# Kernel optimization log

Hardware: AMD Instinct MI355X
Metric: run time of the kernel (lower is better)

The kernel has to match this reference:

```python
import jax, jax.numpy as jnp
import numpy as np

N, E, B, T, H, L = 8192, 2048, 512, 128, 128, 3


def setup_inputs() -> dict:
    key = jax.random.key(0)
    ks = jax.random.split(key, 14)
    # sparse binary hyperedge incidence [E, N]
    Hbat = (jax.random.uniform(ks[0], (E, N)) < 0.01).astype(jnp.float32)
    DV2 = jax.random.uniform(ks[1], (N,)) + 0.1    # D_v^{-1/2} node scaling
    invDE = jax.random.uniform(ks[2], (E,)) + 0.1  # D_e^{-1} edge scaling
    data = jax.random.randint(ks[3], (B, T), 0, N, dtype=jnp.int32)
    lens = jax.random.randint(ks[4], (B,), 1, T + 1, dtype=jnp.int32)
    data_length = jnp.sort(lens)[::-1].at[0].set(T)  # descending, max == T (pack_padded)
    poi = jax.random.normal(ks[5], (N, H), dtype=jnp.float32)
    s = 1.0 / float(np.sqrt(H))
    hgc1_w = jax.random.uniform(ks[6], (H, H), minval=-s, maxval=s)
    hgc1_b = jax.random.uniform(ks[7], (H,), minval=-s, maxval=s)
    hgc2_w = jax.random.uniform(ks[8], (H, H), minval=-s, maxval=s)
    hgc2_b = jax.random.uniform(ks[9], (H,), minval=-s, maxval=s)
    Wih = jax.random.uniform(ks[10], (L, 3 * H, H), minval=-s, maxval=s)
    Whh = jax.random.uniform(ks[11], (L, 3 * H, H), minval=-s, maxval=s)
    bih = jax.random.uniform(ks[12], (L, 3 * H), minval=-s, maxval=s)
    bhh = jax.random.uniform(ks[13], (L, 3 * H), minval=-s, maxval=s)
    return dict(Hbat=Hbat, DV2=DV2, invDE=invDE, data=data, data_length=data_length,
                poi=poi, hgc1_w=hgc1_w, hgc1_b=hgc1_b, hgc2_w=hgc2_w, hgc2_b=hgc2_b,
                Wih=Wih, Whh=Whh, bih=bih, bhh=bhh)


def _gru(x, Wih, Whh, bih, bhh):
    # torch nn.GRU (batch_first, 1 layer, h0=0). x: [B,T,H] -> [B,T,H]
    gx = jnp.einsum('bth,gh->btg', x, Wih) + bih  # precompute input gates [B,T,3H]

    def step(h, gxt):
        gh = h @ Whh.T + bhh
        xr, xz, xn = jnp.split(gxt, 3, axis=-1)
        hr, hz, hn = jnp.split(gh, 3, axis=-1)
        r = jax.nn.sigmoid(xr + hr)
        z = jax.nn.sigmoid(xz + hz)
        n = jnp.tanh(xn + r * hn)
        h_new = (1.0 - z) * n + z * h
        return h_new, h_new

    h0 = jnp.zeros((x.shape[0], x.shape[2]), x.dtype)
    _, ys = jax.lax.scan(step, h0, jnp.swapaxes(gx, 0, 1))
    return jnp.swapaxes(ys, 0, 1)


def reference(Hbat, DV2, invDE, data, data_length, poi,
              hgc1_w, hgc1_b, hgc2_w, hgc2_b, Wih, Whh, bih, bhh):
    # G = diag(DV2) Hbat^T diag(invDE) Hbat diag(DV2); diag_embed GEMMs == row/col scaling
    G = (DV2[:, None] * Hbat.T) @ (invDE[:, None] * Hbat * DV2[None, :])  # [N,N]
    x = jax.nn.relu(G @ (poi @ hgc1_w + hgc1_b)) + poi
    x = G @ (x @ hgc2_w + hgc2_b)
    batch_emb = x[data]  # [B,T,H]
    Tn = batch_emb.shape[1]
    # pad_packed_sequence zero-fills beyond each sequence's length
    mask = (jnp.arange(Tn)[None, :] < data_length[:, None])[:, :, None].astype(batch_emb.dtype)
    inp = batch_emb
    n_layers = Wih.shape[0]
    for l in range(n_layers - 1):
        out = _gru(inp, Wih[l], Whh[l], bih[l], bhh[l]) * mask
        inp = batch_emb + jax.nn.relu(out)
    out = _gru(inp, Wih[-1], Whh[-1], bih[-1], bhh[-1]) * mask
    last = out[jnp.arange(out.shape[0]), data_length - 1]  # gather last valid step
    return jnp.tanh(last)
```

## Files before the change

kernel.cpp:

```cpp
#include <hip/hip_runtime.h>

#define NN 8192
#define EE 2048
#define BB 512
#define TT 128
#define HH 128
#define G3 384
#define MAXNNZ 256
#define MAXDEG 96

typedef __attribute__((ext_vector_type(8))) _Float16 f16x8;
typedef __attribute__((ext_vector_type(4))) float f32x4;

__device__ __forceinline__ float sigm(float x){ return 1.0f/(1.0f+__expf(-x)); }
__device__ __forceinline__ float tanhfast(float x){ return 2.0f/(1.0f+__expf(-2.0f*x)) - 1.0f; }

__device__ __forceinline__ void bar_lds(){
  __builtin_amdgcn_sched_barrier(0);
  asm volatile("s_waitcnt lgkmcnt(0)\n\ts_barrier" ::: "memory");
  __builtin_amdgcn_sched_barrier(0);
}

__global__ __launch_bounds__(256)
void build_nnz(const float* __restrict__ Hb, int* __restrict__ idx, int* __restrict__ cnt){
  __shared__ int c;
  const int e = blockIdx.x;
  if (threadIdx.x == 0) c = 0;
  __syncthreads();
  const float* row = Hb + (size_t)e * NN;
  for (int n = threadIdx.x; n < NN; n += 256){
    if (row[n] != 0.0f){
      int p = atomicAdd(&c, 1);
      if (p < MAXNNZ) idx[e*MAXNNZ + p] = n;
    }
  }
  __syncthreads();
  if (threadIdx.x == 0) cnt[e] = (c < MAXNNZ ? c : MAXNNZ);
}

__global__ __launch_bounds__(128)
void build_nodelists(const int* __restrict__ idx, const int* __restrict__ cnt,
                     int* __restrict__ ndeg, int* __restrict__ nidx){
  const int e = blockIdx.x;
  const int c = cnt[e];
  for (int k = threadIdx.x; k < c; k += 128){
    int n = idx[e*MAXNNZ + k];
    int p = atomicAdd(&ndeg[n], 1);
    if (p < MAXDEG) nidx[n*MAXDEG + p] = e;
  }
}

__global__ __launch_bounds__(256)
void prep_w(const float* __restrict__ W, _Float16* __restrict__ whi,
            _Float16* __restrict__ wlo, int n){
  int i = blockIdx.x*256 + threadIdx.x;
  if (i >= n) return;
  float g = W[i] * 16.0f;
  _Float16 h = (_Float16)g;
  whi[i] = h;
  wlo[i] = (_Float16)(g - (float)h);
}

__global__ __launch_bounds__(256)
void prep_split(const float* __restrict__ X, _Float16* __restrict__ hi,
                _Float16* __restrict__ lo, int n){
  int i = blockIdx.x*256 + threadIdx.x;
  if (i >= n) return;
  float v = X[i];
  _Float16 h = (_Float16)v;
  hi[i] = h;
  lo[i] = (_Float16)(v - (float)h);
}

__global__ __launch_bounds__(256)
void prep_wt(const float* __restrict__ W, _Float16* __restrict__ wt_hi,
             _Float16* __restrict__ wt_lo){
  int i = blockIdx.x*256 + threadIdx.x;
  int k = i >> 7, j = i & 127;
  float g = W[i] * 16.0f;
  _Float16 h = (_Float16)g;
  wt_hi[j*HH + k] = h;
  wt_lo[j*HH + k] = (_Float16)(g - (float)h);
}

template<bool SCALE>
__global__ __launch_bounds__(256)
void mm128_mfma(const _Float16* __restrict__ Ahi, const _Float16* __restrict__ Alo,
                const _Float16* __restrict__ Bh, const _Float16* __restrict__ Bl,
                const float* __restrict__ bias, const float* __restrict__ rowscale,
                float* __restrict__ C)
{
  const int tid = threadIdx.x;
  const int w = tid >> 6, l = tid & 63;
  const int lm = l & 15, q = l >> 4;
  const int r0 = blockIdx.x * 32;
  const int n0 = w * 32;

  f32x4 acc[2][2];
  #pragma unroll
  for (int m=0;m<2;m++)
    #pragma unroll
    for (int n=0;n<2;n++) acc[m][n] = (f32x4){0.f,0.f,0.f,0.f};

  #pragma unroll 2
  for (int ks = 0; ks < 4; ++ks){
    const int kb = ks*32 + q*8;
    f16x8 ah[2], al[2];
    #pragma unroll
    for (int m=0;m<2;m++){
      const size_t ro = (size_t)(r0 + m*16 + lm)*HH + kb;
      ah[m] = *(const f16x8*)(Ahi + ro);
      al[m] = *(const f16x8*)(Alo + ro);
    }
    #pragma unroll
    for (int n=0;n<2;n++){
      const int j = n0 + n*16 + lm;
      f16x8 bh = *(const f16x8*)(Bh + (size_t)j*HH + kb);
      f16x8 bl = *(const f16x8*)(Bl + (size_t)j*HH + kb);
      #pragma unroll
      for (int m=0;m<2;m++){
        acc[m][n] = __builtin_amdgcn_mfma_f32_16x16x32_f16(ah[m], bh, acc[m][n], 0,0,0);
        acc[m][n] = __builtin_amdgcn_mfma_f32_16x16x32_f16(al[m], bh, acc[m][n], 0,0,0);
        acc[m][n] = __builtin_amdgcn_mfma_f32_16x16x32_f16(ah[m], bl, acc[m][n], 0,0,0);
      }
    }
  }
  #pragma unroll
  for (int n=0;n<2;n++){
    const int j = n0 + n*16 + lm;
    const float bv = bias[j];
    #pragma unroll
    for (int m=0;m<2;m++){
      #pragma unroll
      for (int i=0;i<4;i++){
        int r = r0 + m*16 + q*4 + i;
        float cv = acc[m][n][i]*(1.0f/16.0f) + bv;
        if (SCALE) cv *= rowscale[r];
        C[(size_t)r*HH + j] = cv;
      }
    }
  }
}

__global__ __launch_bounds__(128)
void edge_gather(const float* __restrict__ Xs, const int* __restrict__ idx,
                 const int* __restrict__ cnt, const float* __restrict__ invDE,
                 float* __restrict__ Eb){
  __shared__ int sidx[MAXNNZ];
  const int e = blockIdx.x, h = threadIdx.x;
  const int c = cnt[e];
  for (int k = h; k < c; k += 128) sidx[k] = idx[e*MAXNNZ + k];
  __syncthreads();
  float acc = 0.0f;
  int k = 0;
  for (; k + 4 <= c; k += 4){
    float a0 = Xs[(size_t)sidx[k+0]*HH + h];
    float a1 = Xs[(size_t)sidx[k+1]*HH + h];
    float a2 = Xs[(size_t)sidx[k+2]*HH + h];
    float a3 = Xs[(size_t)sidx[k+3]*HH + h];
    acc += (a0 + a1) + (a2 + a3);
  }
  for (; k < c; ++k) acc += Xs[(size_t)sidx[k]*HH + h];
  Eb[e*HH + h] = invDE[e] * acc;
}

template<int MODE>
__global__ __launch_bounds__(128)
void node_gather(const float* __restrict__ Eb, const int* __restrict__ nidx,
                 const int* __restrict__ ndeg, const float* __restrict__ DV2,
                 const float* __restrict__ poi, _Float16* __restrict__ ohi,
                 _Float16* __restrict__ olo, float* __restrict__ Xo){
  __shared__ int sidx[MAXDEG];
  const int n = blockIdx.x, h = threadIdx.x;
  int c = ndeg[n]; c = c < MAXDEG ? c : MAXDEG;
  for (int k = h; k < c; k += 128) sidx[k] = nidx[n*MAXDEG + k];
  __syncthreads();
  float acc = 0.0f;
  int k = 0;
  for (; k + 4 <= c; k += 4){
    float a0 = Eb[(size_t)sidx[k+0]*HH + h];
    float a1 = Eb[(size_t)sidx[k+1]*HH + h];
    float a2 = Eb[(size_t)sidx[k+2]*HH + h];
    float a3 = Eb[(size_t)sidx[k+3]*HH + h];
    acc += (a0 + a1) + (a2 + a3);
  }
  for (; k < c; ++k) acc += Eb[(size_t)sidx[k]*HH + h];
  float v = DV2[n] * acc;
  if (MODE == 1){
    float val = fmaxf(v, 0.0f) + poi[(size_t)n*HH + h];
    _Float16 hh = (_Float16)val;
    ohi[(size_t)n*HH + h] = hh;
    olo[(size_t)n*HH + h] = (_Float16)(val - (float)hh);
  } else {
    Xo[(size_t)n*HH + h] = v;
  }
}

__global__ __launch_bounds__(256)
void gather_emb(const float* __restrict__ X, const int* __restrict__ data,
                float* __restrict__ emb, _Float16* __restrict__ aHi,
                _Float16* __restrict__ aLo){
  int r = blockIdx.x*2 + (threadIdx.x >> 7);
  int h = threadIdx.x & 127;
  int n = data[r];
  float v = X[(size_t)n*HH + h];
  size_t o = (size_t)r*HH + h;
  emb[o] = v;
  _Float16 hh = (_Float16)v;
  aHi[o] = hh;
  aLo[o] = (_Float16)(v - (float)hh);
}

__global__ __launch_bounds__(256)
void gx_gemm(const _Float16* __restrict__ Ahi, const _Float16* __restrict__ Alo,
             const _Float16* __restrict__ Whi, const _Float16* __restrict__ Wlo,
             const float* __restrict__ bih, const int* __restrict__ lens,
             float* __restrict__ gx)
{
  const int blk = blockIdx.x;
  const int b = blk >> 2, tt = blk & 3;
  const int lenb = lens[b];
  if (tt*32 >= lenb) return;
  const int tid = threadIdx.x;
  const int w = tid >> 6, l = tid & 63;
  const int lm = l & 15, q = l >> 4;
  const int r0 = b*TT + tt*32;
  const int n0 = w*96;

  f32x4 acc[2][6];
  #pragma unroll
  for (int m=0;m<2;m++)
    #pragma unroll
    for (int n=0;n<6;n++) acc[m][n] = (f32x4){0.f,0.f,0.f,0.f};

  #pragma unroll 2
  for (int ks = 0; ks < 4; ++ks){
    const int kb = ks*32 + q*8;
    f16x8 ah[2], al[2];
    #pragma unroll
    for (int m=0;m<2;m++){
      const size_t ro = (size_t)(r0 + m*16 + lm)*HH + kb;
      ah[m] = *(const f16x8*)(Ahi + ro);
      al[m] = *(const f16x8*)(Alo + ro);
    }
    #pragma unroll
    for (int n=0;n<6;n++){
      const int g = n0 + n*16 + lm;
      f16x8 bh = *(const f16x8*)(Whi + (size_t)g*HH + kb);
      f16x8 bl = *(const f16x8*)(Wlo + (size_t)g*HH + kb);
      #pragma unroll
      for (int m=0;m<2;m++){
        acc[m][n] = __builtin_amdgcn_mfma_f32_16x16x32_f16(ah[m], bh, acc[m][n], 0,0,0);
        acc[m][n] = __builtin_amdgcn_mfma_f32_16x16x32_f16(al[m], bh, acc[m][n], 0,0,0);
        acc[m][n] = __builtin_amdgcn_mfma_f32_16x16x32_f16(ah[m], bl, acc[m][n], 0,0,0);
      }
    }
  }
  #pragma unroll
  for (int n=0;n<6;n++){
    const int g = n0 + n*16 + lm;
    const float bv = bih[g];
    #pragma unroll
    for (int m=0;m<2;m++){
      #pragma unroll
      for (int i=0;i<4;i++){
        int t = tt*32 + m*16 + q*4 + i;
        gx[((size_t)b*TT + t)*G3 + g] = acc[m][n][i]*(1.0f/16.0f) + bv;
      }
    }
  }
}

template<bool FINAL>
__global__ __launch_bounds__(512, 1)
void gru_scan3(const float* __restrict__ gxp, const float* __restrict__ Whh,
               const float* __restrict__ bhh, const int* __restrict__ lens,
               const float* __restrict__ emb, _Float16* __restrict__ aHi,
               _Float16* __restrict__ aLo, float* __restrict__ final_out)
{
  __shared__ _Float16 hbuf[2][16*HH];
  __shared__ float ghT[2][392];
  const int tid = threadIdx.x;
  const int w = tid >> 6, lane = tid & 63;
  const int lm = lane & 15, q = lane >> 4;
  const int b0 = blockIdx.x * 2;

  f16x8 wf[3][4];
  #pragma unroll
  for (int n=0; n<3; ++n){
    const int col = w*48 + n*16 + lm;
    const float* wr = Whh + (size_t)col*HH;
    #pragma unroll
    for (int ks=0; ks<4; ++ks){
      const int kb = ks*32 + q*8;
      float4 f0 = *(const float4*)(wr + kb);
      float4 f1 = *(const float4*)(wr + kb + 4);
      float fv[8] = {f0.x,f0.y,f0.z,f0.w,f1.x,f1.y,f1.z,f1.w};
      union { f16x8 v; _Float16 u[8]; } uu;
      #pragma unroll
      for (int j=0;j<8;j++) uu.u[j] = (_Float16)(fv[j] * 16.0f);
      wf[n][ks] = uu.v;
    }
  }
  const float S = 1.0f/16.0f;
  const int lenmax = lens[b0];

  const int gb = tid >> 7, gd = tid & 127;
  float bR=0.f, bZ=0.f, bN=0.f; int glen=0;
  const float* gxrow = nullptr;
  const float* erow = nullptr;
  _Float16 *ahrow = nullptr, *alrow = nullptr;
  if (tid < 256){
    bR = bhh[gd]; bZ = bhh[HH+gd]; bN = bhh[2*HH+gd];
    glen = lens[b0+gb];
    gxrow = gxp + (size_t)(b0+gb)*TT*G3;
    if (!FINAL){
      erow  = emb + (size_t)(b0+gb)*TT*HH + gd;
      ahrow = aHi + (size_t)(b0+gb)*TT*HH + gd;
      alrow = aLo + (size_t)(b0+gb)*TT*HH + gd;
    }
  }

  {
    unsigned int* z = (unsigned int*)&hbuf[0][0];
    #pragma unroll 1
    for (int i = tid; i < 2*16*HH/2; i += 512) z[i] = 0u;
  }
  __syncthreads();

  float xv0=0.f, xv1=0.f, xv2=0.f, xe=0.f, hp=0.f;
  if (tid < 256){
    xv0 = gxrow[gd]; xv1 = gxrow[128+gd]; xv2 = gxrow[256+gd];
    if (!FINAL) xe = erow[0];
  }

  int cur = 0;
  #pragma unroll 1
  for (int t = 0; t < lenmax; ++t){
    f16x8 av[4];
    #pragma unroll
    for (int ks=0; ks<4; ++ks){
      int off = (lm*256 + ks*64 + q*16) ^ ((lm & 7) << 4);
      av[ks] = *(const f16x8*)((const char*)&hbuf[cur][0] + off);
    }
    float xn0=0.f, xn1=0.f, xn2=0.f, xen=0.f;
    if (tid < 256){
      int tp = (t+1 < lenmax) ? t+1 : t;
      const float* bgx = gxrow + (size_t)tp*G3;
      xn0 = bgx[gd]; xn1 = bgx[128+gd]; xn2 = bgx[256+gd];
      if (!FINAL) xen = erow[(size_t)tp*HH];
    }
    f32x4 a0 = (f32x4){0.f,0.f,0.f,0.f}, a1 = a0, a2 = a0;
    #pragma unroll
    for (int ks=0; ks<4; ++ks){
      a0 = __builtin_amdgcn_mfma_f32_16x16x32_f16(av[ks], wf[0][ks], a0, 0,0,0);
      a1 = __builtin_amdgcn_mfma_f32_16x16x32_f16(av[ks], wf[1][ks], a1, 0,0,0);
      a2 = __builtin_amdgcn_mfma_f32_16x16x32_f16(av[ks], wf[2][ks], a2, 0,0,0);
    }
    if (q == 0){
      const int c0 = w*48 + lm;
      ghT[0][c0]      = a0[0];  ghT[1][c0]      = a0[1];
      ghT[0][c0+16]   = a1[0];  ghT[1][c0+16]   = a1[1];
      ghT[0][c0+32]   = a2[0];  ghT[1][c0+32]   = a2[1];
    }
    bar_lds();

    if (tid < 256){
      float gr = ghT[gb][gd], gz = ghT[gb][128+gd], gn = ghT[gb][256+gd];
      float r = sigm(xv0 + gr*S + bR);
      float z = sigm(xv1 + gz*S + bZ);
      float n = tanhfast(xv2 + r*(gn*S + bN));
      float hnew = (1.0f - z)*n + z*hp;
      hp = hnew;
      int off = (gb*256 + gd*2) ^ (gb << 4);
      *(_Float16*)((char*)&hbuf[cur^1][0] + off) = (_Float16)hnew;
      if (!FINAL){
        float a = xe + fmaxf(hnew, 0.0f);
        _Float16 ah = (_Float16)a;
        ahrow[(size_t)t*HH] = ah;
        alrow[(size_t)t*HH] = (_Float16)(a - (float)ah);
      } else {
        if (t == glen - 1)
          final_out[(size_t)(b0+gb)*HH + gd] = tanhfast(hnew);
      }
    }
    xv0 = xn0; xv1 = xn1; xv2 = xn2; xe = xen;
    bar_lds();
    cur ^= 1;
  }
}

extern "C" void kernel_launch(void* const* d_in, const int* in_sizes, int n_in,
                              void* d_out, int out_size, void* d_ws, size_t ws_size,
                              hipStream_t stream)
{
  const float* Hb    = (const float*)d_in[0];
  const float* DV2   = (const float*)d_in[1];
  const float* invDE = (const float*)d_in[2];
  const int*   data  = (const int*)d_in[3];
  const int*   dlen  = (const int*)d_in[4];
  const float* poi   = (const float*)d_in[5];
  const float* w1    = (const float*)d_in[6];
  const float* b1    = (const float*)d_in[7];
  const float* w2    = (const float*)d_in[8];
  const float* b2    = (const float*)d_in[9];
  const float* Wih   = (const float*)d_in[10];
  const float* Whh   = (const float*)d_in[11];
  const float* bih   = (const float*)d_in[12];
  const float* bhh   = (const float*)d_in[13];
  float* out = (float*)d_out;

  float* ws   = (float*)d_ws;
  float* x1s  = ws;
  float* x3s  = x1s + (size_t)NN*HH;
  float* x4   = x3s + (size_t)NN*HH;
  float* ebuf = x4  + (size_t)NN*HH;
  float* gx   = ebuf + (size_t)EE*HH;
  float* emb  = gx  + (size_t)BB*TT*G3;
  _Float16* aHi  = (_Float16*)(emb + (size_t)BB*TT*HH);
  _Float16* aLo  = aHi + (size_t)BB*TT*HH;
  _Float16* x2hi = aLo + (size_t)BB*TT*HH;
  _Float16* x2lo = x2hi + (size_t)NN*HH;
  _Float16* pHi  = x2lo + (size_t)NN*HH;
  _Float16* pLo  = pHi + (size_t)NN*HH;
  _Float16* Whi  = pLo + (size_t)NN*HH;
  _Float16* Wlo  = Whi + (size_t)3*G3*HH;
  _Float16* w1th = Wlo + (size_t)3*G3*HH;
  _Float16* w1tl = w1th + (size_t)HH*HH;
  _Float16* w2th = w1tl + (size_t)HH*HH;
  _Float16* w2tl = w2th + (size_t)HH*HH;
  int* idx  = (int*)(w2tl + (size_t)HH*HH);
  int* cnt  = idx + (size_t)EE*MAXNNZ;
  int* ndeg = cnt + EE;
  int* nidx = ndeg + NN;

  hipMemsetAsync(ndeg, 0, NN*sizeof(int), stream);
  build_nnz<<<EE, 256, 0, stream>>>(Hb, idx, cnt);
  build_nodelists<<<EE, 128, 0, stream>>>(idx, cnt, ndeg, nidx);
  prep_w<<<(3*G3*HH + 255)/256, 256, 0, stream>>>(Wih, Whi, Wlo, 3*G3*HH);
  prep_wt<<<HH*HH/256, 256, 0, stream>>>(w1, w1th, w1tl);
  prep_wt<<<HH*HH/256, 256, 0, stream>>>(w2, w2th, w2tl);
  prep_split<<<NN*HH/256, 256, 0, stream>>>(poi, pHi, pLo, NN*HH);

  mm128_mfma<true><<<NN/32, 256, 0, stream>>>(pHi, pLo, w1th, w1tl, b1, DV2, x1s);
  edge_gather<<<EE, 128, 0, stream>>>(x1s, idx, cnt, invDE, ebuf);
  node_gather<1><<<NN, 128, 0, stream>>>(ebuf, nidx, ndeg, DV2, poi, x2hi, x2lo, (float*)nullptr);
  mm128_mfma<true><<<NN/32, 256, 0, stream>>>(x2hi, x2lo, w2th, w2tl, b2, DV2, x3s);
  edge_gather<<<EE, 128, 0, stream>>>(x3s, idx, cnt, invDE, ebuf);
  node_gather<2><<<NN, 128, 0, stream>>>(ebuf, nidx, ndeg, DV2, (const float*)nullptr,
                                         (_Float16*)nullptr, (_Float16*)nullptr, x4);
  gather_emb<<<BB*TT/2, 256, 0, stream>>>(x4, data, emb, aHi, aLo);

  for (int l = 0; l < 3; ++l){
    gx_gemm<<<BB*4, 256, 0, stream>>>(aHi, aLo, Whi + (size_t)l*G3*HH,
        Wlo + (size_t)l*G3*HH, bih + (size_t)l*G3, dlen, gx);
    if (l < 2)
      gru_scan3<false><<<BB/2, 512, 0, stream>>>(gx, Whh + (size_t)l*G3*HH,
          bhh + (size_t)l*G3, dlen, emb, aHi, aLo, (float*)nullptr);
    else
      gru_scan3<true><<<BB/2, 512, 0, stream>>>(gx, Whh + (size_t)l*G3*HH,
          bhh + (size_t)l*G3, dlen, (const float*)nullptr,
          (_Float16*)nullptr, (_Float16*)nullptr, out);
  }
}
```

Before: 580.4 us.

## Remap GRU scan columns per wave to drop LDS gate exchange barrier

The recurrent weights are remapped so each wave's three MFMA tiles hold the r, z and n gates for the same 16 hidden dims. The gate math can then run straight from the MFMA accumulators, which removes the ghT shared-memory exchange and one barrier per timestep. The final output write is deferred until after the loop. The gx GEMM is also retiled to 64 timesteps per block with a per-row length guard, trading fewer blocks for more accumulator registers.

```diff
diff --git a/kernel.cpp b/kernel.cpp
--- a/kernel.cpp
+++ b/kernel.cpp
@@ -218,27 +218,27 @@
              float* __restrict__ gx)
 {
   const int blk = blockIdx.x;
-  const int b = blk >> 2, tt = blk & 3;
+  const int b = blk >> 1, tt = blk & 1;
   const int lenb = lens[b];
-  if (tt*32 >= lenb) return;
+  if (tt*64 >= lenb) return;
   const int tid = threadIdx.x;
   const int w = tid >> 6, l = tid & 63;
   const int lm = l & 15, q = l >> 4;
-  const int r0 = b*TT + tt*32;
+  const int r0 = b*TT + tt*64;
   const int n0 = w*96;
 
-  f32x4 acc[2][6];
+  f32x4 acc[4][6];
   #pragma unroll
-  for (int m=0;m<2;m++)
+  for (int m=0;m<4;m++)
     #pragma unroll
     for (int n=0;n<6;n++) acc[m][n] = (f32x4){0.f,0.f,0.f,0.f};
 
   #pragma unroll 2
   for (int ks = 0; ks < 4; ++ks){
     const int kb = ks*32 + q*8;
-    f16x8 ah[2], al[2];
-    #pragma unroll
-    for (int m=0;m<2;m++){
+    f16x8 ah[4], al[4];
+    #pragma unroll
+    for (int m=0;m<4;m++){
       const size_t ro = (size_t)(r0 + m*16 + lm)*HH + kb;
       ah[m] = *(const f16x8*)(Ahi + ro);
       al[m] = *(const f16x8*)(Alo + ro);
@@ -249,7 +249,7 @@
       f16x8 bh = *(const f16x8*)(Whi + (size_t)g*HH + kb);
       f16x8 bl = *(const f16x8*)(Wlo + (size_t)g*HH + kb);
       #pragma unroll
-      for (int m=0;m<2;m++){
+      for (int m=0;m<4;m++){
         acc[m][n] = __builtin_amdgcn_mfma_f32_16x16x32_f16(ah[m], bh, acc[m][n], 0,0,0);
         acc[m][n] = __builtin_amdgcn_mfma_f32_16x16x32_f16(al[m], bh, acc[m][n], 0,0,0);
         acc[m][n] = __builtin_amdgcn_mfma_f32_16x16x32_f16(ah[m], bl, acc[m][n], 0,0,0);
@@ -261,11 +261,12 @@
     const int g = n0 + n*16 + lm;
     const float bv = bih[g];
     #pragma unroll
-    for (int m=0;m<2;m++){
+    for (int m=0;m<4;m++){
       #pragma unroll
       for (int i=0;i<4;i++){
-        int t = tt*32 + m*16 + q*4 + i;
-        gx[((size_t)b*TT + t)*G3 + g] = acc[m][n][i]*(1.0f/16.0f) + bv;
+        int t = tt*64 + m*16 + q*4 + i;
+        if (t < lenb)
+          gx[((size_t)b*TT + t)*G3 + g] = acc[m][n][i]*(1.0f/16.0f) + bv;
       }
     }
   }
@@ -273,23 +274,22 @@
 
 template<bool FINAL>
 __global__ __launch_bounds__(512, 1)
-void gru_scan3(const float* __restrict__ gxp, const float* __restrict__ Whh,
+void gru_scan4(const float* __restrict__ gxp, const float* __restrict__ Whh,
                const float* __restrict__ bhh, const int* __restrict__ lens,
                const float* __restrict__ emb, _Float16* __restrict__ aHi,
                _Float16* __restrict__ aLo, float* __restrict__ final_out)
 {
   __shared__ _Float16 hbuf[2][16*HH];
-  __shared__ float ghT[2][392];
   const int tid = threadIdx.x;
   const int w = tid >> 6, lane = tid & 63;
   const int lm = lane & 15, q = lane >> 4;
   const int b0 = blockIdx.x * 2;
+  const int d = w*16 + lm;
 
   f16x8 wf[3][4];
   #pragma unroll
-  for (int n=0; n<3; ++n){
-    const int col = w*48 + n*16 + lm;
-    const float* wr = Whh + (size_t)col*HH;
+  for (int g=0; g<3; ++g){
+    const float* wr = Whh + (size_t)(g*HH + d)*HH;
     #pragma unroll
     for (int ks=0; ks<4; ++ks){
       const int kb = ks*32 + q*8;
@@ -299,26 +299,22 @@
       union { f16x8 v; _Float16 u[8]; } uu;
       #pragma unroll
       for (int j=0;j<8;j++) uu.u[j] = (_Float16)(fv[j] * 16.0f);
-      wf[n][ks] = uu.v;
+      wf[g][ks] = uu.v;
     }
   }
   const float S = 1.0f/16.0f;
   const int lenmax = lens[b0];
-
-  const int gb = tid >> 7, gd = tid & 127;
-  float bR=0.f, bZ=0.f, bN=0.f; int glen=0;
-  const float* gxrow = nullptr;
-  const float* erow = nullptr;
-  _Float16 *ahrow = nullptr, *alrow = nullptr;
-  if (tid < 256){
-    bR = bhh[gd]; bZ = bhh[HH+gd]; bN = bhh[2*HH+gd];
-    glen = lens[b0+gb];
-    gxrow = gxp + (size_t)(b0+gb)*TT*G3;
-    if (!FINAL){
-      erow  = emb + (size_t)(b0+gb)*TT*HH + gd;
-      ahrow = aHi + (size_t)(b0+gb)*TT*HH + gd;
-      alrow = aLo + (size_t)(b0+gb)*TT*HH + gd;
-    }
+  const int len0 = lens[b0], len1 = lens[b0+1];
+  const float bR = bhh[d], bZ = bhh[HH+d], bN = bhh[2*HH+d];
+  const float* gx0 = gxp + (size_t)b0*TT*G3 + d;
+  const float* gx1 = gxp + (size_t)(b0+1)*TT*G3 + d;
+  const float* e0 = nullptr; const float* e1 = nullptr;
+  _Float16 *ah0=nullptr,*al0=nullptr,*ah1=nullptr,*al1=nullptr;
+  if (!FINAL){
+    e0  = emb + (size_t)b0*TT*HH + d;
+    e1  = emb + (size_t)(b0+1)*TT*HH + d;
+    ah0 = aHi + (size_t)b0*TT*HH + d;      al0 = aLo + (size_t)b0*TT*HH + d;
+    ah1 = aHi + (size_t)(b0+1)*TT*HH + d;  al1 = aLo + (size_t)(b0+1)*TT*HH + d;
   }
 
   {
@@ -328,10 +324,13 @@
   }
   __syncthreads();
 
-  float xv0=0.f, xv1=0.f, xv2=0.f, xe=0.f, hp=0.f;
-  if (tid < 256){
-    xv0 = gxrow[gd]; xv1 = gxrow[128+gd]; xv2 = gxrow[256+gd];
-    if (!FINAL) xe = erow[0];
+  float hp0=0.f, hp1=0.f, fo0=0.f, fo1=0.f;
+  float xv[6] = {0,0,0,0,0,0};
+  float xe0=0.f, xe1=0.f;
+  if (q == 0){
+    xv[0]=gx0[0]; xv[1]=gx0[128]; xv[2]=gx0[256];
+    xv[3]=gx1[0]; xv[4]=gx1[128]; xv[5]=gx1[256];
+    if (!FINAL){ xe0 = e0[0]; xe1 = e1[0]; }
   }
 
   int cur = 0;
@@ -343,50 +342,56 @@
       int off = (lm*256 + ks*64 + q*16) ^ ((lm & 7) << 4);
       av[ks] = *(const f16x8*)((const char*)&hbuf[cur][0] + off);
     }
-    float xn0=0.f, xn1=0.f, xn2=0.f, xen=0.f;
-    if (tid < 256){
+    float xn[6] = {0,0,0,0,0,0};
+    float xen0=0.f, xen1=0.f;
+    if (q == 0){
       int tp = (t+1 < lenmax) ? t+1 : t;
-      const float* bgx = gxrow + (size_t)tp*G3;
-      xn0 = bgx[gd]; xn1 = bgx[128+gd]; xn2 = bgx[256+gd];
-      if (!FINAL) xen = erow[(size_t)tp*HH];
-    }
-    f32x4 a0 = (f32x4){0.f,0.f,0.f,0.f}, a1 = a0, a2 = a0;
+      const float* g0 = gx0 + (size_t)tp*G3;
+      const float* g1 = gx1 + (size_t)tp*G3;
+      xn[0]=g0[0]; xn[1]=g0[128]; xn[2]=g0[256];
+      xn[3]=g1[0]; xn[4]=g1[128]; xn[5]=g1[256];
+      if (!FINAL){ xen0 = e0[(size_t)tp*HH]; xen1 = e1[(size_t)tp*HH]; }
+    }
+    f32x4 aR = (f32x4){0.f,0.f,0.f,0.f}, aZ = aR, aN = aR;
     #pragma unroll
     for (int ks=0; ks<4; ++ks){
-      a0 = __builtin_amdgcn_mfma_f32_16x16x32_f16(av[ks], wf[0][ks], a0, 0,0,0);
-      a1 = __builtin_amdgcn_mfma_f32_16x16x32_f16(av[ks], wf[1][ks], a1, 0,0,0);
-      a2 = __builtin_amdgcn_mfma_f32_16x16x32_f16(av[ks], wf[2][ks], a2, 0,0,0);
+      aR = __builtin_amdgcn_mfma_f32_16x16x32_f16(av[ks], wf[0][ks], aR, 0,0,0);
+      aZ = __builtin_amdgcn_mfma_f32_16x16x32_f16(av[ks], wf[1][ks], aZ, 0,0,0);
+      aN = __builtin_amdgcn_mfma_f32_16x16x32_f16(av[ks], wf[2][ks], aN, 0,0,0);
     }
     if (q == 0){
-      const int c0 = w*48 + lm;
-      ghT[0][c0]      = a0[0];  ghT[1][c0]      = a0[1];
-      ghT[0][c0+16]   = a1[0];  ghT[1][c0+16]   = a1[1];
-      ghT[0][c0+32]   = a2[0];  ghT[1][c0+32]   = a2[1];
-    }
-    bar_lds();
-
-    if (tid < 256){
-      float gr = ghT[gb][gd], gz = ghT[gb][128+gd], gn = ghT[gb][256+gd];
-      float r = sigm(xv0 + gr*S + bR);
-      float z = sigm(xv1 + gz*S + bZ);
-      float n = tanhfast(xv2 + r*(gn*S + bN));
-      float hnew = (1.0f - z)*n + z*hp;
-      hp = hnew;
-      int off = (gb*256 + gd*2) ^ (gb << 4);
-      *(_Float16*)((char*)&hbuf[cur^1][0] + off) = (_Float16)hnew;
+      float r0 = sigm(xv[0] + aR[0]*S + bR);
+      float z0 = sigm(xv[1] + aZ[0]*S + bZ);
+      float n0 = tanhfast(xv[2] + r0*(aN[0]*S + bN));
+      float h0 = (1.0f - z0)*n0 + z0*hp0; hp0 = h0;
+      float r1 = sigm(xv[3] + aR[1]*S + bR);
+      float z1 = sigm(xv[4] + aZ[1]*S + bZ);
+      float n1 = tanhfast(xv[5] + r1*(aN[1]*S + bN));
+      float h1 = (1.0f - z1)*n1 + z1*hp1; hp1 = h1;
+      char* hb = (char*)&hbuf[cur^1][0];
+      *(_Float16*)(hb + (d*2))                 = (_Float16)h0;
+      *(_Float16*)(hb + 256 + ((d*2) ^ 16))    = (_Float16)h1;
       if (!FINAL){
-        float a = xe + fmaxf(hnew, 0.0f);
-        _Float16 ah = (_Float16)a;
-        ahrow[(size_t)t*HH] = ah;
-        alrow[(size_t)t*HH] = (_Float16)(a - (float)ah);
+        float a0v = xe0 + fmaxf(h0, 0.0f);
+        _Float16 a0h = (_Float16)a0v;
+        ah0[(size_t)t*HH] = a0h;  al0[(size_t)t*HH] = (_Float16)(a0v - (float)a0h);
+        float a1v = xe1 + fmaxf(h1, 0.0f);
+        _Float16 a1h = (_Float16)a1v;
+        ah1[(size_t)t*HH] = a1h;  al1[(size_t)t*HH] = (_Float16)(a1v - (float)a1h);
       } else {
-        if (t == glen - 1)
-          final_out[(size_t)(b0+gb)*HH + gd] = tanhfast(hnew);
+        if (t == len0 - 1) fo0 = tanhfast(h0);
+        if (t == len1 - 1) fo1 = tanhfast(h1);
       }
     }
-    xv0 = xn0; xv1 = xn1; xv2 = xn2; xe = xen;
+    #pragma unroll
+    for (int k2=0;k2<6;k2++) xv[k2] = xn[k2];
+    xe0 = xen0; xe1 = xen1;
     bar_lds();
     cur ^= 1;
+  }
+  if (FINAL && q == 0){
+    final_out[(size_t)b0*HH + d]     = fo0;
+    final_out[(size_t)(b0+1)*HH + d] = fo1;
   }
 }
 
@@ -452,13 +457,13 @@
   gather_emb<<<BB*TT/2, 256, 0, stream>>>(x4, data, emb, aHi, aLo);
 
   for (int l = 0; l < 3; ++l){
-    gx_gemm<<<BB*4, 256, 0, stream>>>(aHi, aLo, Whi + (size_t)l*G3*HH,
+    gx_gemm<<<BB*2, 256, 0, stream>>>(aHi, aLo, Whi + (size_t)l*G3*HH,
         Wlo + (size_t)l*G3*HH, bih + (size_t)l*G3, dlen, gx);
     if (l < 2)
-      gru_scan3<false><<<BB/2, 512, 0, stream>>>(gx, Whh + (size_t)l*G3*HH,
+      gru_scan4<false><<<BB/2, 512, 0, stream>>>(gx, Whh + (size_t)l*G3*HH,
           bhh + (size_t)l*G3, dlen, emb, aHi, aLo, (float*)nullptr);
     else
-      gru_scan3<true><<<BB/2, 512, 0, stream>>>(gx, Whh + (size_t)l*G3*HH,
+      gru_scan4<true><<<BB/2, 512, 0, stream>>>(gx, Whh + (size_t)l*G3*HH,
           bhh + (size_t)l*G3, dlen, (const float*)nullptr,
           (_Float16*)nullptr, (_Float16*)nullptr, out);
   }
```

New measurement: 682.9 us. +17.7%, slower.

## Run GRU scan with one sequence per block and enlarge gx GEMM row tiles

Applied to the files above, without the earlier changes.

The GRU recurrent kernel now processes one batch sequence per 256-thread block instead of two per 512-thread block. Each wave holds six Whh fragments and loops only to that sequence's own length, so short sequences no longer wait on the longest in a pair, and two blocks can share a CU. The gx GEMM tile grows from 32 to 64 timesteps per block, with stores past the sequence length skipped. The costs are more registers per wave, half the MFMA rows left unused per step since only one row of the 16-row tile is live, and coarser GEMM blocks.

```diff
diff --git a/kernel.cpp b/kernel.cpp
--- a/kernel.cpp
+++ b/kernel.cpp
@@ -218,27 +218,27 @@
              float* __restrict__ gx)
 {
   const int blk = blockIdx.x;
-  const int b = blk >> 2, tt = blk & 3;
+  const int b = blk >> 1, tt = blk & 1;
   const int lenb = lens[b];
-  if (tt*32 >= lenb) return;
+  if (tt*64 >= lenb) return;
   const int tid = threadIdx.x;
   const int w = tid >> 6, l = tid & 63;
   const int lm = l & 15, q = l >> 4;
-  const int r0 = b*TT + tt*32;
+  const int r0 = b*TT + tt*64;
   const int n0 = w*96;
 
-  f32x4 acc[2][6];
+  f32x4 acc[4][6];
   #pragma unroll
-  for (int m=0;m<2;m++)
+  for (int m=0;m<4;m++)
     #pragma unroll
     for (int n=0;n<6;n++) acc[m][n] = (f32x4){0.f,0.f,0.f,0.f};
 
   #pragma unroll 2
   for (int ks = 0; ks < 4; ++ks){
     const int kb = ks*32 + q*8;
-    f16x8 ah[2], al[2];
-    #pragma unroll
-    for (int m=0;m<2;m++){
+    f16x8 ah[4], al[4];
+    #pragma unroll
+    for (int m=0;m<4;m++){
       const size_t ro = (size_t)(r0 + m*16 + lm)*HH + kb;
       ah[m] = *(const f16x8*)(Ahi + ro);
       al[m] = *(const f16x8*)(Alo + ro);
@@ -249,7 +249,7 @@
       f16x8 bh = *(const f16x8*)(Whi + (size_t)g*HH + kb);
       f16x8 bl = *(const f16x8*)(Wlo + (size_t)g*HH + kb);
       #pragma unroll
-      for (int m=0;m<2;m++){
+      for (int m=0;m<4;m++){
         acc[m][n] = __builtin_amdgcn_mfma_f32_16x16x32_f16(ah[m], bh, acc[m][n], 0,0,0);
         acc[m][n] = __builtin_amdgcn_mfma_f32_16x16x32_f16(al[m], bh, acc[m][n], 0,0,0);
         acc[m][n] = __builtin_amdgcn_mfma_f32_16x16x32_f16(ah[m], bl, acc[m][n], 0,0,0);
@@ -261,34 +261,35 @@
     const int g = n0 + n*16 + lm;
     const float bv = bih[g];
     #pragma unroll
-    for (int m=0;m<2;m++){
+    for (int m=0;m<4;m++){
       #pragma unroll
       for (int i=0;i<4;i++){
-        int t = tt*32 + m*16 + q*4 + i;
-        gx[((size_t)b*TT + t)*G3 + g] = acc[m][n][i]*(1.0f/16.0f) + bv;
+        int t = tt*64 + m*16 + q*4 + i;
+        if (t < lenb)
+          gx[((size_t)b*TT + t)*G3 + g] = acc[m][n][i]*(1.0f/16.0f) + bv;
       }
     }
   }
 }
 
 template<bool FINAL>
-__global__ __launch_bounds__(512, 1)
-void gru_scan3(const float* __restrict__ gxp, const float* __restrict__ Whh,
+__global__ __launch_bounds__(256, 2)
+void gru_scan5(const float* __restrict__ gxp, const float* __restrict__ Whh,
                const float* __restrict__ bhh, const int* __restrict__ lens,
                const float* __restrict__ emb, _Float16* __restrict__ aHi,
                _Float16* __restrict__ aLo, float* __restrict__ final_out)
 {
   __shared__ _Float16 hbuf[2][16*HH];
-  __shared__ float ghT[2][392];
+  __shared__ float ghT[G3 + 8];
   const int tid = threadIdx.x;
   const int w = tid >> 6, lane = tid & 63;
   const int lm = lane & 15, q = lane >> 4;
-  const int b0 = blockIdx.x * 2;
-
-  f16x8 wf[3][4];
+  const int b = blockIdx.x;
+
+  f16x8 wf[6][4];
   #pragma unroll
-  for (int n=0; n<3; ++n){
-    const int col = w*48 + n*16 + lm;
+  for (int n=0; n<6; ++n){
+    const int col = w*96 + n*16 + lm;
     const float* wr = Whh + (size_t)col*HH;
     #pragma unroll
     for (int ks=0; ks<4; ++ks){
@@ -303,40 +304,39 @@
     }
   }
   const float S = 1.0f/16.0f;
-  const int lenmax = lens[b0];
-
-  const int gb = tid >> 7, gd = tid & 127;
-  float bR=0.f, bZ=0.f, bN=0.f; int glen=0;
+  const int lenb = lens[b];
+
+  const int gd = tid & 127;
+  float bR=0.f, bZ=0.f, bN=0.f;
   const float* gxrow = nullptr;
   const float* erow = nullptr;
   _Float16 *ahrow = nullptr, *alrow = nullptr;
-  if (tid < 256){
+  if (tid < 128){
     bR = bhh[gd]; bZ = bhh[HH+gd]; bN = bhh[2*HH+gd];
-    glen = lens[b0+gb];
-    gxrow = gxp + (size_t)(b0+gb)*TT*G3;
+    gxrow = gxp + (size_t)b*TT*G3;
     if (!FINAL){
-      erow  = emb + (size_t)(b0+gb)*TT*HH + gd;
-      ahrow = aHi + (size_t)(b0+gb)*TT*HH + gd;
-      alrow = aLo + (size_t)(b0+gb)*TT*HH + gd;
+      erow  = emb + (size_t)b*TT*HH + gd;
+      ahrow = aHi + (size_t)b*TT*HH + gd;
+      alrow = aLo + (size_t)b*TT*HH + gd;
     }
   }
 
   {
     unsigned int* z = (unsigned int*)&hbuf[0][0];
     #pragma unroll 1
-    for (int i = tid; i < 2*16*HH/2; i += 512) z[i] = 0u;
+    for (int i = tid; i < 2*16*HH/2; i += 256) z[i] = 0u;
   }
   __syncthreads();
 
-  float xv0=0.f, xv1=0.f, xv2=0.f, xe=0.f, hp=0.f;
-  if (tid < 256){
+  float xv0=0.f, xv1=0.f, xv2=0.f, xe=0.f, hp=0.f, fo=0.f;
+  if (tid < 128){
     xv0 = gxrow[gd]; xv1 = gxrow[128+gd]; xv2 = gxrow[256+gd];
     if (!FINAL) xe = erow[0];
   }
 
   int cur = 0;
   #pragma unroll 1
-  for (int t = 0; t < lenmax; ++t){
+  for (int t = 0; t < lenb; ++t){
     f16x8 av[4];
     #pragma unroll
     for (int ks=0; ks<4; ++ks){
@@ -344,50 +344,51 @@
       av[ks] = *(const f16x8*)((const char*)&hbuf[cur][0] + off);
     }
     float xn0=0.f, xn1=0.f, xn2=0.f, xen=0.f;
-    if (tid < 256){
-      int tp = (t+1 < lenmax) ? t+1 : t;
+    if (tid < 128){
+      int tp = (t+1 < lenb) ? t+1 : t;
       const float* bgx = gxrow + (size_t)tp*G3;
       xn0 = bgx[gd]; xn1 = bgx[128+gd]; xn2 = bgx[256+gd];
       if (!FINAL) xen = erow[(size_t)tp*HH];
     }
-    f32x4 a0 = (f32x4){0.f,0.f,0.f,0.f}, a1 = a0, a2 = a0;
+    f32x4 a[6];
+    #pragma unroll
+    for (int n=0;n<6;n++) a[n] = (f32x4){0.f,0.f,0.f,0.f};
     #pragma unroll
     for (int ks=0; ks<4; ++ks){
-      a0 = __builtin_amdgcn_mfma_f32_16x16x32_f16(av[ks], wf[0][ks], a0, 0,0,0);
-      a1 = __builtin_amdgcn_mfma_f32_16x16x32_f16(av[ks], wf[1][ks], a1, 0,0,0);
-      a2 = __builtin_amdgcn_mfma_f32_16x16x32_f16(av[ks], wf[2][ks], a2, 0,0,0);
+      #pragma unroll
+      for (int n=0;n<6;n++)
+        a[n] = __builtin_amdgcn_mfma_f32_16x16x32_f16(av[ks], wf[n][ks], a[n], 0,0,0);
     }
     if (q == 0){
-      const int c0 = w*48 + lm;
-      ghT[0][c0]      = a0[0];  ghT[1][c0]      = a0[1];
-      ghT[0][c0+16]   = a1[0];  ghT[1][c0+16]   = a1[1];
-      ghT[0][c0+32]   = a2[0];  ghT[1][c0+32]   = a2[1];
+      const int c0 = w*96 + lm;
+      #pragma unroll
+      for (int n=0;n<6;n++) ghT[c0 + n*16] = a[n][0];
     }
     bar_lds();
 
-    if (tid < 256){
-      float gr = ghT[gb][gd], gz = ghT[gb][128+gd], gn = ghT[gb][256+gd];
+    if (tid < 128){
+      float gr = ghT[gd], gz = ghT[128+gd], gn = ghT[256+gd];
       float r = sigm(xv0 + gr*S + bR);
       float z = sigm(xv1 + gz*S + bZ);
       float n = tanhfast(xv2 + r*(gn*S + bN));
       float hnew = (1.0f - z)*n + z*hp;
       hp = hnew;
-      int off = (gb*256 + gd*2) ^ (gb << 4);
-      *(_Float16*)((char*)&hbuf[cur^1][0] + off) = (_Float16)hnew;
+      *(_Float16*)((char*)&hbuf[cur^1][0] + gd*2) = (_Float16)hnew;
       if (!FINAL){
-        float a = xe + fmaxf(hnew, 0.0f);
-        _Float16 ah = (_Float16)a;
+        float av_ = xe + fmaxf(hnew, 0.0f);
+        _Float16 ah = (_Float16)av_;
         ahrow[(size_t)t*HH] = ah;
-        alrow[(size_t)t*HH] = (_Float16)(a - (float)ah);
+        alrow[(size_t)t*HH] = (_Float16)(av_ - (float)ah);
       } else {
-        if (t == glen - 1)
-          final_out[(size_t)(b0+gb)*HH + gd] = tanhfast(hnew);
+        if (t == lenb - 1) fo = tanhfast(hnew);
       }
     }
     xv0 = xn0; xv1 = xn1; xv2 = xn2; xe = xen;
     bar_lds();
     cur ^= 1;
   }
+  if (FINAL && tid < 128)
+    final_out[(size_t)b*HH + gd] = fo;
 }
 
 extern "C" void kernel_launch(void* const* d_in, const int* in_sizes, int n_in,
@@ -452,13 +453,13 @@
   gather_emb<<<BB*TT/2, 256, 0, stream>>>(x4, data, emb, aHi, aLo);
 
   for (int l = 0; l < 3; ++l){
-    gx_gemm<<<BB*4, 256, 0, stream>>>(aHi, aLo, Whi + (size_t)l*G3*HH,
+    gx_gemm<<<BB*2, 256, 0, stream>>>(aHi, aLo, Whi + (size_t)l*G3*HH,
         Wlo + (size_t)l*G3*HH, bih + (size_t)l*G3, dlen, gx);
     if (l < 2)
-      gru_scan3<false><<<BB/2, 512, 0, stream>>>(gx, Whh + (size_t)l*G3*HH,
+      gru_scan5<false><<<BB, 256, 0, stream>>>(gx, Whh + (size_t)l*G3*HH,
           bhh + (size_t)l*G3, dlen, emb, aHi, aLo, (float*)nullptr);
     else
-      gru_scan3<true><<<BB/2, 512, 0, stream>>>(gx, Whh + (size_t)l*G3*HH,
+      gru_scan5<true><<<BB, 256, 0, stream>>>(gx, Whh + (size_t)l*G3*HH,
           bhh + (size_t)l*G3, dlen, (const float*)nullptr,
           (_Float16*)nullptr, (_Float16*)nullptr, out);
   }
```

After: 638.6 us. 1.1x slower.

## Fuse input-gate GEMM and all three GRU layers into one kernel

Applied to the files above, without the earlier changes.

Replaces the per-layer gx_gemm plus gru_scan launches (six kernels) with a single persistent kernel. Each block computes the input-gate projection for its own two sequences, then runs the recurrent scan, and loops over the three layers internally. The gx results round-trip only within the block's own rows, so no grid-wide sync is needed. This removes launch gaps and inter-kernel dependencies. The cost is that the input GEMM now runs on only 256 blocks, serially before each scan, instead of a wide 2048-block grid.

```diff
diff --git a/kernel.cpp b/kernel.cpp
--- a/kernel.cpp
+++ b/kernel.cpp
@@ -211,72 +211,13 @@
   aLo[o] = (_Float16)(v - (float)hh);
 }
 
-__global__ __launch_bounds__(256)
-void gx_gemm(const _Float16* __restrict__ Ahi, const _Float16* __restrict__ Alo,
-             const _Float16* __restrict__ Whi, const _Float16* __restrict__ Wlo,
-             const float* __restrict__ bih, const int* __restrict__ lens,
-             float* __restrict__ gx)
-{
-  const int blk = blockIdx.x;
-  const int b = blk >> 2, tt = blk & 3;
-  const int lenb = lens[b];
-  if (tt*32 >= lenb) return;
-  const int tid = threadIdx.x;
-  const int w = tid >> 6, l = tid & 63;
-  const int lm = l & 15, q = l >> 4;
-  const int r0 = b*TT + tt*32;
-  const int n0 = w*96;
-
-  f32x4 acc[2][6];
-  #pragma unroll
-  for (int m=0;m<2;m++)
-    #pragma unroll
-    for (int n=0;n<6;n++) acc[m][n] = (f32x4){0.f,0.f,0.f,0.f};
-
-  #pragma unroll 2
-  for (int ks = 0; ks < 4; ++ks){
-    const int kb = ks*32 + q*8;
-    f16x8 ah[2], al[2];
-    #pragma unroll
-    for (int m=0;m<2;m++){
-      const size_t ro = (size_t)(r0 + m*16 + lm)*HH + kb;
-      ah[m] = *(const f16x8*)(Ahi + ro);
-      al[m] = *(const f16x8*)(Alo + ro);
-    }
-    #pragma unroll
-    for (int n=0;n<6;n++){
-      const int g = n0 + n*16 + lm;
-      f16x8 bh = *(const f16x8*)(Whi + (size_t)g*HH + kb);
-      f16x8 bl = *(const f16x8*)(Wlo + (size_t)g*HH + kb);
-      #pragma unroll
-      for (int m=0;m<2;m++){
-        acc[m][n] = __builtin_amdgcn_mfma_f32_16x16x32_f16(ah[m], bh, acc[m][n], 0,0,0);
-        acc[m][n] = __builtin_amdgcn_mfma_f32_16x16x32_f16(al[m], bh, acc[m][n], 0,0,0);
-        acc[m][n] = __builtin_amdgcn_mfma_f32_16x16x32_f16(ah[m], bl, acc[m][n], 0,0,0);
-      }
-    }
-  }
-  #pragma unroll
-  for (int n=0;n<6;n++){
-    const int g = n0 + n*16 + lm;
-    const float bv = bih[g];
-    #pragma unroll
-    for (int m=0;m<2;m++){
-      #pragma unroll
-      for (int i=0;i<4;i++){
-        int t = tt*32 + m*16 + q*4 + i;
-        gx[((size_t)b*TT + t)*G3 + g] = acc[m][n][i]*(1.0f/16.0f) + bv;
-      }
-    }
-  }
-}
-
-template<bool FINAL>
 __global__ __launch_bounds__(512, 1)
-void gru_scan3(const float* __restrict__ gxp, const float* __restrict__ Whh,
-               const float* __restrict__ bhh, const int* __restrict__ lens,
+void gru_fused(const float* __restrict__ WhhAll, const float* __restrict__ bhhAll,
+               const _Float16* __restrict__ WhiAll, const _Float16* __restrict__ WloAll,
+               const float* __restrict__ bihAll, const int* __restrict__ lens,
                const float* __restrict__ emb, _Float16* __restrict__ aHi,
-               _Float16* __restrict__ aLo, float* __restrict__ final_out)
+               _Float16* __restrict__ aLo, float* __restrict__ gxb,
+               float* __restrict__ out)
 {
   __shared__ _Float16 hbuf[2][16*HH];
   __shared__ float ghT[2][392];
@@ -284,109 +225,170 @@
   const int w = tid >> 6, lane = tid & 63;
   const int lm = lane & 15, q = lane >> 4;
   const int b0 = blockIdx.x * 2;
-
-  f16x8 wf[3][4];
-  #pragma unroll
-  for (int n=0; n<3; ++n){
-    const int col = w*48 + n*16 + lm;
-    const float* wr = Whh + (size_t)col*HH;
+  const int n0 = w * 48;
+
+  const int len0 = lens[b0], len1 = lens[b0+1];
+  const int lenmax = len0;
+  const int ntl[2] = {(len0+15)>>4, (len1+15)>>4};
+
+  const int gb = (tid < 256) ? (tid >> 7) : 0;
+  const int gd = tid & 127;
+  const float* gxrow = gxb + (size_t)(b0+gb)*TT*G3;
+  const float* erow  = emb + (size_t)(b0+gb)*TT*HH + gd;
+  _Float16* ahrow = aHi + (size_t)(b0+gb)*TT*HH + gd;
+  _Float16* alrow = aLo + (size_t)(b0+gb)*TT*HH + gd;
+  const int glen = gb ? len1 : len0;
+
+  #pragma unroll 1
+  for (int l = 0; l < 3; ++l){
+    const bool fin = (l == 2);
+    const _Float16* Whi = WhiAll + (size_t)l*G3*HH;
+    const _Float16* Wlo = WloAll + (size_t)l*G3*HH;
+    const float* bih = bihAll + l*G3;
+    const float* Whh = WhhAll + (size_t)l*G3*HH;
+    const float* bhh = bhhAll + l*G3;
+
+    #pragma unroll 1
+    for (int bb = 0; bb < 2; ++bb){
+      const int ntb = ntl[bb];
+      #pragma unroll 1
+      for (int rt = 0; rt < ntb; ++rt){
+        f32x4 acc0 = (f32x4){0.f,0.f,0.f,0.f}, acc1 = acc0, acc2 = acc0;
+        #pragma unroll
+        for (int ks = 0; ks < 4; ++ks){
+          const int kb = ks*32 + q*8;
+          const size_t ro = ((size_t)(b0+bb)*TT + rt*16 + lm)*HH + kb;
+          f16x8 ah = *(const f16x8*)(aHi + ro);
+          f16x8 al = *(const f16x8*)(aLo + ro);
+          {
+            const int g = n0 + lm;
+            f16x8 bh = *(const f16x8*)(Whi + (size_t)g*HH + kb);
+            f16x8 bl = *(const f16x8*)(Wlo + (size_t)g*HH + kb);
+            acc0 = __builtin_amdgcn_mfma_f32_16x16x32_f16(ah, bh, acc0, 0,0,0);
+            acc0 = __builtin_amdgcn_mfma_f32_16x16x32_f16(al, bh, acc0, 0,0,0);
+            acc0 = __builtin_amdgcn_mfma_f32_16x16x32_f16(ah, bl, acc0, 0,0,0);
+          }
+          {
+            const int g = n0 + 16 + lm;
+            f16x8 bh = *(const f16x8*)(Whi + (size_t)g*HH + kb);
+            f16x8 bl = *(const f16x8*)(Wlo + (size_t)g*HH + kb);
+            acc1 = __builtin_amdgcn_mfma_f32_16x16x32_f16(ah, bh, acc1, 0,0,0);
+            acc1 = __builtin_amdgcn_mfma_f32_16x16x32_f16(al, bh, acc1, 0,0,0);
+            acc1 = __builtin_amdgcn_mfma_f32_16x16x32_f16(ah, bl, acc1, 0,0,0);
+          }
+          {
+            const int g = n0 + 32 + lm;
+            f16x8 bh = *(const f16x8*)(Whi + (size_t)g*HH + kb);
+            f16x8 bl = *(const f16x8*)(Wlo + (size_t)g*HH + kb);
+            acc2 = __builtin_amdgcn_mfma_f32_16x16x32_f16(ah, bh, acc2, 0,0,0);
+            acc2 = __builtin_amdgcn_mfma_f32_16x16x32_f16(al, bh, acc2, 0,0,0);
+            acc2 = __builtin_amdgcn_mfma_f32_16x16x32_f16(ah, bl, acc2, 0,0,0);
+          }
+        }
+        float* gout = gxb + ((size_t)(b0+bb)*TT + rt*16)*G3;
+        #pragma unroll
+        for (int i=0;i<4;i++){
+          const int t = q*4 + i;
+          gout[(size_t)t*G3 + n0 + lm]      = acc0[i]*(1.0f/16.0f) + bih[n0 + lm];
+          gout[(size_t)t*G3 + n0 + 16 + lm] = acc1[i]*(1.0f/16.0f) + bih[n0 + 16 + lm];
+          gout[(size_t)t*G3 + n0 + 32 + lm] = acc2[i]*(1.0f/16.0f) + bih[n0 + 32 + lm];
+        }
+      }
+    }
+
+    f16x8 wf[3][4];
     #pragma unroll
-    for (int ks=0; ks<4; ++ks){
-      const int kb = ks*32 + q*8;
-      float4 f0 = *(const float4*)(wr + kb);
-      float4 f1 = *(const float4*)(wr + kb + 4);
-      float fv[8] = {f0.x,f0.y,f0.z,f0.w,f1.x,f1.y,f1.z,f1.w};
-      union { f16x8 v; _Float16 u[8]; } uu;
+    for (int n=0; n<3; ++n){
+      const int col = n0 + n*16 + lm;
+      const float* wr = Whh + (size_t)col*HH;
       #pragma unroll
-      for (int j=0;j<8;j++) uu.u[j] = (_Float16)(fv[j] * 16.0f);
-      wf[n][ks] = uu.v;
-    }
-  }
-  const float S = 1.0f/16.0f;
-  const int lenmax = lens[b0];
-
-  const int gb = tid >> 7, gd = tid & 127;
-  float bR=0.f, bZ=0.f, bN=0.f; int glen=0;
-  const float* gxrow = nullptr;
-  const float* erow = nullptr;
-  _Float16 *ahrow = nullptr, *alrow = nullptr;
-  if (tid < 256){
-    bR = bhh[gd]; bZ = bhh[HH+gd]; bN = bhh[2*HH+gd];
-    glen = lens[b0+gb];
-    gxrow = gxp + (size_t)(b0+gb)*TT*G3;
-    if (!FINAL){
-      erow  = emb + (size_t)(b0+gb)*TT*HH + gd;
-      ahrow = aHi + (size_t)(b0+gb)*TT*HH + gd;
-      alrow = aLo + (size_t)(b0+gb)*TT*HH + gd;
-    }
-  }
-
-  {
-    unsigned int* z = (unsigned int*)&hbuf[0][0];
+      for (int ks=0; ks<4; ++ks){
+        const int kb = ks*32 + q*8;
+        float4 f0 = *(const float4*)(wr + kb);
+        float4 f1 = *(const float4*)(wr + kb + 4);
+        float fv[8] = {f0.x,f0.y,f0.z,f0.w,f1.x,f1.y,f1.z,f1.w};
+        union { f16x8 v; _Float16 u[8]; } uu;
+        #pragma unroll
+        for (int j=0;j<8;j++) uu.u[j] = (_Float16)(fv[j] * 16.0f);
+        wf[n][ks] = uu.v;
+      }
+    }
+    const float S = 1.0f/16.0f;
+    const float bR = bhh[gd], bZ = bhh[HH+gd], bN = bhh[2*HH+gd];
+
+    {
+      unsigned int* z = (unsigned int*)&hbuf[0][0];
+      #pragma unroll 1
+      for (int i = tid; i < 2*16*HH/2; i += 512) z[i] = 0u;
+    }
+    __syncthreads();
+
+    float xv0=0.f, xv1=0.f, xv2=0.f, xe=0.f, hp=0.f, fo=0.f;
+    if (tid < 256){
+      xv0 = gxrow[gd]; xv1 = gxrow[128+gd]; xv2 = gxrow[256+gd];
+      if (!fin) xe = erow[0];
+    }
+
+    int cur = 0;
     #pragma unroll 1
-    for (int i = tid; i < 2*16*HH/2; i += 512) z[i] = 0u;
-  }
-  __syncthreads();
-
-  float xv0=0.f, xv1=0.f, xv2=0.f, xe=0.f, hp=0.f;
-  if (tid < 256){
-    xv0 = gxrow[gd]; xv1 = gxrow[128+gd]; xv2 = gxrow[256+gd];
-    if (!FINAL) xe = erow[0];
-  }
-
-  int cur = 0;
-  #pragma unroll 1
-  for (int t = 0; t < lenmax; ++t){
-    f16x8 av[4];
-    #pragma unroll
-    for (int ks=0; ks<4; ++ks){
-      int off = (lm*256 + ks*64 + q*16) ^ ((lm & 7) << 4);
-      av[ks] = *(const f16x8*)((const char*)&hbuf[cur][0] + off);
-    }
-    float xn0=0.f, xn1=0.f, xn2=0.f, xen=0.f;
-    if (tid < 256){
-      int tp = (t+1 < lenmax) ? t+1 : t;
-      const float* bgx = gxrow + (size_t)tp*G3;
-      xn0 = bgx[gd]; xn1 = bgx[128+gd]; xn2 = bgx[256+gd];
-      if (!FINAL) xen = erow[(size_t)tp*HH];
-    }
-    f32x4 a0 = (f32x4){0.f,0.f,0.f,0.f}, a1 = a0, a2 = a0;
-    #pragma unroll
-    for (int ks=0; ks<4; ++ks){
-      a0 = __builtin_amdgcn_mfma_f32_16x16x32_f16(av[ks], wf[0][ks], a0, 0,0,0);
-      a1 = __builtin_amdgcn_mfma_f32_16x16x32_f16(av[ks], wf[1][ks], a1, 0,0,0);
-      a2 = __builtin_amdgcn_mfma_f32_16x16x32_f16(av[ks], wf[2][ks], a2, 0,0,0);
-    }
-    if (q == 0){
-      const int c0 = w*48 + lm;
-      ghT[0][c0]      = a0[0];  ghT[1][c0]      = a0[1];
-      ghT[0][c0+16]   = a1[0];  ghT[1][c0+16]   = a1[1];
-      ghT[0][c0+32]   = a2[0];  ghT[1][c0+32]   = a2[1];
-    }
-    bar_lds();
-
-    if (tid < 256){
-      float gr = ghT[gb][gd], gz = ghT[gb][128+gd], gn = ghT[gb][256+gd];
-      float r = sigm(xv0 + gr*S + bR);
-      float z = sigm(xv1 + gz*S + bZ);
-      float n = tanhfast(xv2 + r*(gn*S + bN));
-      float hnew = (1.0f - z)*n + z*hp;
-      hp = hnew;
-      int off = (gb*256 + gd*2) ^ (gb << 4);
-      *(_Float16*)((char*)&hbuf[cur^1][0] + off) = (_Float16)hnew;
-      if (!FINAL){
-        float a = xe + fmaxf(hnew, 0.0f);
-        _Float16 ah = (_Float16)a;
-        ahrow[(size_t)t*HH] = ah;
-        alrow[(size_t)t*HH] = (_Float16)(a - (float)ah);
-      } else {
-        if (t == glen - 1)
-          final_out[(size_t)(b0+gb)*HH + gd] = tanhfast(hnew);
-      }
-    }
-    xv0 = xn0; xv1 = xn1; xv2 = xn2; xe = xen;
-    bar_lds();
-    cur ^= 1;
+    for (int t = 0; t < lenmax; ++t){
+      f16x8 av[4];
+      #pragma unroll
+      for (int ks=0; ks<4; ++ks){
+        int off = (lm*256 + ks*64 + q*16) ^ ((lm & 7) << 4);
+        av[ks] = *(const f16x8*)((const char*)&hbuf[cur][0] + off);
+      }
+      float xn0=0.f, xn1=0.f, xn2=0.f, xen=0.f;
+      if (tid < 256){
+        int tp = (t+1 < lenmax) ? t+1 : t;
+        const float* bgx = gxrow + (size_t)tp*G3;
+        xn0 = bgx[gd]; xn1 = bgx[128+gd]; xn2 = bgx[256+gd];
+        if (!fin) xen = erow[(size_t)tp*HH];
+      }
+      f32x4 a0 = (f32x4){0.f,0.f,0.f,0.f}, a1 = a0, a2 = a0;
+      #pragma unroll
+      for (int ks=0; ks<4; ++ks){
+        a0 = __builtin_amdgcn_mfma_f32_16x16x32_f16(av[ks], wf[0][ks], a0, 0,0,0);
+        a1 = __builtin_amdgcn_mfma_f32_16x16x32_f16(av[ks], wf[1][ks], a1, 0,0,0);
+        a2 = __builtin_amdgcn_mfma_f32_16x16x32_f16(av[ks], wf[2][ks], a2, 0,0,0);
+      }
+      if (q == 0){
+        const int c0 = n0 + lm;
+        ghT[0][c0]      = a0[0];  ghT[1][c0]      = a0[1];
+        ghT[0][c0+16]   = a1[0];  ghT[1][c0+16]   = a1[1];
+        ghT[0][c0+32]   = a2[0];  ghT[1][c0+32]   = a2[1];
+      }
+      bar_lds();
+
+      if (tid < 256){
+        float gr = ghT[gb][gd], gz = ghT[gb][128+gd], gn = ghT[gb][256+gd];
+        float r = sigm(xv0 + gr*S + bR);
+        float z = sigm(xv1 + gz*S + bZ);
+        float n = tanhfast(xv2 + r*(gn*S + bN));
+        float hnew = (1.0f - z)*n + z*hp;
+        hp = hnew;
+        int off = (gb*256 + gd*2) ^ (gb << 4);
+        *(_Float16*)((char*)&hbuf[cur^1][0] + off) = (_Float16)hnew;
+        if (!fin){
+          float a = xe + fmaxf(hnew, 0.0f);
+          _Float16 ah = (_Float16)a;
+          ahrow[(size_t)t*HH] = ah;
+          alrow[(size_t)t*HH] = (_Float16)(a - (float)ah);
+        } else {
+          if (t == glen - 1) fo = tanhfast(hnew);
+        }
+      }
+      xv0 = xn0; xv1 = xn1; xv2 = xn2; xe = xen;
+      bar_lds();
+      cur ^= 1;
+    }
+
+    if (fin){
+      if (tid < 256)
+        out[(size_t)(b0+gb)*HH + gd] = fo;
+    } else {
+      __syncthreads();
+    }
   }
 }
 
@@ -451,15 +453,6 @@
                                          (_Float16*)nullptr, (_Float16*)nullptr, x4);
   gather_emb<<<BB*TT/2, 256, 0, stream>>>(x4, data, emb, aHi, aLo);
 
-  for (int l = 0; l < 3; ++l){
-    gx_gemm<<<BB*4, 256, 0, stream>>>(aHi, aLo, Whi + (size_t)l*G3*HH,
-        Wlo + (size_t)l*G3*HH, bih + (size_t)l*G3, dlen, gx);
-    if (l < 2)
-      gru_scan3<false><<<BB/2, 512, 0, stream>>>(gx, Whh + (size_t)l*G3*HH,
-          bhh + (size_t)l*G3, dlen, emb, aHi, aLo, (float*)nullptr);
-    else
-      gru_scan3<true><<<BB/2, 512, 0, stream>>>(gx, Whh + (size_t)l*G3*HH,
-          bhh + (size_t)l*G3, dlen, (const float*)nullptr,
-          (_Float16*)nullptr, (_Float16*)nullptr, out);
-  }
-}
+  gru_fused<<<BB/2, 512, 0, stream>>>(Whh, bhh, Whi, Wlo, bih, dlen,
+                                      emb, aHi, aLo, gx, out);
+}
```

After: 495.2 us. 14.7% less time.
